# Kernel optimization log

Measured on AMD Instinct MI355X. Metric: run time of the kernel, lower is better.

Reference implementation:

```python
import jax, jax.numpy as jnp
import numpy as np

MS = [1, 2, 4, 8, 16]          # args.ms_token_size
RESI = 0.5                     # Phi resi_ratio
# PhiPartiallyShared: 4 phis, ticks = linspace(1/(2*4)... wait K==4 -> linspace(1/3/K, 1-1/3/K, K)
_TICKS = np.linspace(1.0 / 3.0 / 4.0, 1.0 - 1.0 / 3.0 / 4.0, 4)
PHI_IDX = [int(np.argmin(np.abs(_TICKS - (si / (len(MS) - 1))))) for si in range(len(MS))]


def _phi(h, w, b):
    # Phi.forward: h*(1-r) + conv3x3(h)*r
    c = jax.lax.conv_general_dilated(h, w, (1, 1), 'SAME',
                                     dimension_numbers=('NCHW', 'OIHW', 'NCHW'))
    c = c + b[None, :, None, None]
    return h * (1.0 - RESI) + c * RESI


def _area_down(z, ph, pw):
    # F.interpolate mode='area' with integer ratio == block mean
    B, C, H, W = z.shape
    return z.reshape(B, C, ph, H // ph, pw, W // pw).mean(axis=(3, 5))


def setup_inputs() -> dict:
    key = jax.random.key(0)
    k1, k2, k3 = jax.random.split(key, 3)
    B, C, H, W = 32, 64, 16, 16
    K = 8192
    f = jax.random.normal(k1, (B, C, H, W), dtype=jnp.float32)
    # nn.Embedding init: uniform(-1/K, 1/K)
    emb_w = jax.random.uniform(k2, (K, C), dtype=jnp.float32,
                               minval=-1.0 / K, maxval=1.0 / K)
    phi_w = jax.random.normal(k3, (4, C, C, 3, 3), dtype=jnp.float32) * 0.02
    phi_b = jnp.zeros((4, C), dtype=jnp.float32)
    return {'f': f, 'emb_w': emb_w, 'phi_w': phi_w, 'phi_b': phi_b}


def reference(f, emb_w, phi_w, phi_b):
    B, C, H, W = f.shape
    f = jax.lax.stop_gradient(f)  # z_enc.detach()
    z_rest = f
    f_hat = jnp.zeros_like(f)
    w_sq = jnp.sum(emb_w * emb_w, axis=1)  # [K]
    for si, pn in enumerate(MS):
        last = (si == len(MS) - 1)
        z = z_rest if last else _area_down(z_rest, pn, pn)
        zf = z.transpose(0, 2, 3, 1).reshape(-1, C)  # [B*pn*pn, C]
        # ||z||^2 + ||w||^2 - 2 z.w  (matches square-sum + addmm)
        d = jnp.sum(zf * zf, axis=1, keepdims=True) + w_sq[None, :] \
            - 2.0 * (zf @ emb_w.T)
        tok = jnp.argmin(d, axis=1)                  # [B*pn*pn]
        h = emb_w[tok].reshape(B, pn, pn, C).transpose(0, 3, 1, 2)
        if not last:
            h = jax.image.resize(h, (B, C, H, W), method='cubic')
        h = _phi(h, phi_w[PHI_IDX[si]], phi_b[PHI_IDX[si]])
        f_hat = f_hat + h
        z_rest = z_rest - h
    return f_hat
```

## Files before the change

### kernel.cpp

```cpp
#include <hip/hip_runtime.h>
#include <math.h>
#include <float.h>

#define BB 32
#define CC 64
#define KK 8192
#define NPIX 256
#define NELEM (BB*CC*NPIX)

typedef unsigned short u16;
typedef __attribute__((ext_vector_type(8))) short bf16x8;
typedef __attribute__((ext_vector_type(4))) float f32x4;

__device__ __forceinline__ u16 f2bf(float v) {
  unsigned u = __float_as_uint(v);
  return (u16)((u + 0x7FFFu + ((u >> 16) & 1u)) >> 16);
}

__global__ void k_prep(const float* __restrict__ f, float* __restrict__ zr,
                       float* __restrict__ out, const float* __restrict__ emb,
                       float* __restrict__ wsq32, u16* __restrict__ ehi) {
  int i = blockIdx.x * 256 + threadIdx.x;
  if (i < NELEM) { zr[i] = f[i]; out[i] = 0.f; ehi[i] = f2bf(emb[i]); }
  if (i < KK) {
    const float* row = emb + i * 64;
    double s = 0.0;
    #pragma unroll
    for (int c = 0; c < 64; ++c) s += (double)row[c] * (double)row[c];
    wsq32[i] = (float)s;
  }
}

__global__ void k_down(const float* __restrict__ zr, float* __restrict__ zd, int pn) {
#pragma clang fp contract(off)
  int i = blockIdx.x * 256 + threadIdx.x;
  int pnpn = pn * pn;
  int n = BB * CC * pnpn;
  if (i >= n) return;
  int x = i % pn; int y = (i / pn) % pn; int bc = i / pnpn;
  int bs = 16 / pn;
  const float* src = zr + bc * NPIX + (y * bs) * 16 + x * bs;
  float acc = 0.f;
  for (int dy = 0; dy < bs; ++dy) {
    const float* a = src + dy * 16;
    float s;
    if (bs == 16) {
      float r[8];
      #pragma unroll
      for (int j = 0; j < 8; ++j) r[j] = a[j] + a[8 + j];
      s = ((r[0] + r[1]) + (r[2] + r[3])) + ((r[4] + r[5]) + (r[6] + r[7]));
    } else if (bs == 8) {
      s = ((a[0] + a[1]) + (a[2] + a[3])) + ((a[4] + a[5]) + (a[6] + a[7]));
    } else if (bs == 4) {
      s = ((a[0] + a[1]) + a[2]) + a[3];
    } else {
      s = a[0] + a[1];
    }
    acc = acc + s;
  }
  zd[i] = acc * (1.f / (bs * bs));
}

__global__ __launch_bounds__(256) void k_pack(
    const float* __restrict__ zr, int pn, int bs,
    u16* __restrict__ zhi, float* __restrict__ zt32, float* __restrict__ zsq32) {
#pragma clang fp contract(off)
  int tid = threadIdx.x;
  int lv = tid >> 6, c = tid & 63;
  int vec = blockIdx.x * 4 + lv;
  int pnpn = pn * pn;
  int b = vec / pnpn, p = vec % pnpn;
  int y = p / pn, x = p % pn;
  const float* src = zr + ((size_t)(b * 64 + c)) * 256 + (y * bs) * 16 + x * bs;
  float v;
  if (bs == 1) {
    v = src[0];
  } else {
    v = (src[0] + src[1]) + (src[16] + src[17]);
    v = v * 0.25f;
  }
  zhi[(size_t)vec * 64 + c] = f2bf(v);
  zt32[(size_t)vec * 64 + c] = v;
  double sq = (double)v * (double)v;
  #pragma unroll
  for (int m = 1; m < 64; m <<= 1)
    sq += __shfl_xor(sq, m, 64);
  if (c == 0) zsq32[vec] = (float)sq;
}

__global__ __launch_bounds__(256, 4) void k_argmin(
    const float* __restrict__ zd, const float* __restrict__ emb,
    const float* __restrict__ wsq32,
    float* __restrict__ pd, int* __restrict__ pi,
    int numVec, int pnpn, int kchunk) {
#pragma clang fp contract(off)
  __shared__ __align__(16) float zt[32][68];
  __shared__ __align__(16) float et[64 * 64];
  __shared__ float ws_s[64];
  __shared__ float red_d[256];
  __shared__ int   red_i[256];
  int tid = threadIdx.x;
  int v0 = blockIdx.x * 32;
  int kbase = blockIdx.y * kchunk;

  for (int idx = tid; idx < 32 * 64; idx += 256) {
    int v = idx >> 6, c = idx & 63;
    int vi = v0 + v;
    float val = 0.f;
    if (vi < numVec) {
      int b = vi / pnpn, p = vi % pnpn;
      val = zd[(b * 64 + c) * pnpn + p];
    }
    zt[v][c] = val;
  }
  __syncthreads();

  const int v = tid & 31, kg = tid >> 5;
  float4 z4[16];
  #pragma unroll
  for (int i = 0; i < 16; ++i) z4[i] = *reinterpret_cast<float4*>(&zt[v][i * 4]);
  float zsq = 0.f;
  #pragma unroll
  for (int i = 0; i < 16; ++i)
    zsq += z4[i].x * z4[i].x + z4[i].y * z4[i].y + z4[i].z * z4[i].z + z4[i].w * z4[i].w;

  float bd = FLT_MAX; int bi = 0x7fffffff;
  for (int k0 = 0; k0 < kchunk; k0 += 64) {
    __syncthreads();
    {
      const float4* gsrc = reinterpret_cast<const float4*>(emb + (size_t)(kbase + k0) * 64);
      float4* ldst = reinterpret_cast<float4*>(et);
      #pragma unroll
      for (int idx = 0; idx < 4; ++idx)
        ldst[tid + idx * 256] = gsrc[tid + idx * 256];
    }
    if (tid < 64) ws_s[tid] = wsq32[kbase + k0 + tid];
    __syncthreads();
    #pragma unroll
    for (int j = 0; j < 8; ++j) {
      int kl = kg * 8 + j;
      const float4* e4 = reinterpret_cast<const float4*>(&et[kl * 64]);
      float acc = 0.f;
      #pragma unroll
      for (int i = 0; i < 16; ++i) {
        float4 e = e4[i];
        acc = __builtin_fmaf(z4[i].x, e.x, acc);
        acc = __builtin_fmaf(z4[i].y, e.y, acc);
        acc = __builtin_fmaf(z4[i].z, e.z, acc);
        acc = __builtin_fmaf(z4[i].w, e.w, acc);
      }
      float t1 = zsq + ws_s[kl];
      float d  = t1 - 2.0f * acc;
      if (d < bd) { bd = d; bi = kbase + k0 + kl; }
    }
  }
  red_d[tid] = bd; red_i[tid] = bi;
  __syncthreads();
  if (tid < 32) {
    float fb = red_d[tid]; int fi = red_i[tid];
    #pragma unroll
    for (int g = 1; g < 8; ++g) {
      float cd = red_d[g * 32 + tid]; int ci = red_i[g * 32 + tid];
      if (cd < fb || (cd == fb && ci < fi)) { fb = cd; fi = ci; }
    }
    int vi = v0 + tid;
    if (vi < numVec) {
      pd[blockIdx.y * numVec + vi] = fb;
      pi[blockIdx.y * numVec + vi] = fi;
    }
  }
}

__global__ __launch_bounds__(256, 8) void k_argmin_mfma(
    const u16* __restrict__ zhi, const u16* __restrict__ ehi,
    const float* __restrict__ wsq32, float* __restrict__ cdp,
    int numVec, int part) {
  __shared__ u16  es[2][64 * 72];
  __shared__ float wss[2][64];
  const int tid = threadIdx.x;
  const int wid = tid >> 6, lane = tid & 63;
  const int l15 = lane & 15, l4 = lane >> 4;
  const int vw = blockIdx.x * 128 + wid * 32;
  const int kbase = blockIdx.y * part;
  const int KSx = gridDim.y;

  bf16x8 za[2][2];
  #pragma unroll
  for (int s = 0; s < 2; ++s) {
    const u16* zp = zhi + (size_t)(vw + s * 16 + l15) * 64 + l4 * 8;
    za[s][0] = *reinterpret_cast<const bf16x8*>(zp);
    za[s][1] = *reinterpret_cast<const bf16x8*>(zp + 32);
  }

  float d1[2][4], d2[2][4];
  #pragma unroll
  for (int s = 0; s < 2; ++s)
    #pragma unroll
    for (int r = 0; r < 4; ++r) { d1[s][r] = -FLT_MAX; d2[s][r] = -FLT_MAX; }

  const int NT = part >> 6;
  #define STAGE(buf, t)                                                      \
    { const u16* src = ehi + (size_t)(kbase + (t) * 64) * 64;                \
      int code = tid >> 2, seg = tid & 3;                                    \
      const bf16x8* s8 = reinterpret_cast<const bf16x8*>(src + code * 64 + seg * 16); \
      bf16x8 v0 = s8[0], v1 = s8[1];                                         \
      bf16x8* d8 = reinterpret_cast<bf16x8*>(&es[buf][code * 72 + seg * 16]);\
      d8[0] = v0; d8[1] = v1;                                                \
      if (tid < 64) wss[buf][tid] = wsq32[kbase + (t) * 64 + tid]; }

  STAGE(0, 0);
  __syncthreads();
  for (int t = 0; t < NT; ++t) {
    int cur = t & 1;
    if (t + 1 < NT) { STAGE(cur ^ 1, t + 1); }
    #pragma unroll
    for (int ct = 0; ct < 4; ++ct) {
      const u16* eb = &es[cur][(ct * 16 + l15) * 72 + l4 * 8];
      bf16x8 b0 = *reinterpret_cast<const bf16x8*>(eb);
      bf16x8 b1 = *reinterpret_cast<const bf16x8*>(eb + 32);
      float hwl = -0.5f * wss[cur][ct * 16 + l15];
      unsigned idu = (unsigned)(t * 64 + ct * 16 + l15);
      #pragma unroll
      for (int s = 0; s < 2; ++s) {
        f32x4 acc = {hwl, hwl, hwl, hwl};
        acc = __builtin_amdgcn_mfma_f32_16x16x32_bf16(za[s][0], b0, acc, 0, 0, 0);
        acc = __builtin_amdgcn_mfma_f32_16x16x32_bf16(za[s][1], b1, acc, 0, 0, 0);
        #pragma unroll
        for (int r = 0; r < 4; ++r) {
          float key = __uint_as_float((__float_as_uint(acc[r]) & 0xFFFFFF00u) | idu);
          float o1 = d1[s][r];
          d1[s][r] = fmaxf(o1, key);
          d2[s][r] = __builtin_amdgcn_fmed3f(o1, key, d2[s][r]);
        }
      }
    }
    __syncthreads();
  }

  #pragma unroll
  for (int s = 0; s < 2; ++s)
    #pragma unroll
    for (int r = 0; r < 4; ++r) {
      float q0 = d1[s][r], q1 = d2[s][r];
      #pragma unroll
      for (int m = 1; m < 8; m <<= 1) {
        float p0 = __shfl_xor(q0, m), p1 = __shfl_xor(q1, m);
        { bool c0 = p0 > q0, c1 = p0 > q1;
          q1 = c0 ? q0 : (c1 ? p0 : q1);
          q0 = c0 ? p0 : q0; }
        { bool c0 = p1 > q0, c1 = p1 > q1;
          q1 = c0 ? q0 : (c1 ? p1 : q1);
          q0 = c0 ? p1 : q0; }
      }
      if ((l15 & 7) == 0) {
        int vec = vw + s * 16 + l4 * 4 + r;
        int half = l15 >> 3;
        size_t base = ((size_t)vec * KSx + blockIdx.y) * 4 + half * 2;
        cdp[base + 0] = q0; cdp[base + 1] = q1;
      }
    }
}

__global__ __launch_bounds__(256) void k_rescore(
    const float* __restrict__ cdp, const float* __restrict__ zt32,
    const float* __restrict__ emb, const float* __restrict__ wsq32,
    const float* __restrict__ zsq32,
    float* __restrict__ pd, int* __restrict__ pi,
    int numVec, int ncand) {
#pragma clang fp contract(off)
  __shared__ float zsh[4][64];
  int tid = threadIdx.x;
  int wid = tid >> 6, lane = tid & 63;
  int v0 = blockIdx.x * 4;
  zsh[wid][lane] = zt32[(size_t)v0 * 64 + tid];
  __syncthreads();

  int vec = v0 + wid;
  float zsq = zsq32[vec];
  const float* cdb = cdp + (size_t)vec * ncand;
  float dv0 = cdb[lane];
  float dv1 = (ncand > 64) ? cdb[lane + 64] : -FLT_MAX;
  int j0 = lane, j1 = lane + 64;
  int ki0 = ((j0 >> 2) << 8) | (int)(__float_as_uint(dv0) & 0xFFu);
  int ki1 = ((j1 >> 2) << 8) | (int)(__float_as_uint(dv1) & 0xFFu);

  float amax = fmaxf(dv0, dv1);
  #pragma unroll
  for (int m = 1; m < 64; m <<= 1) amax = fmaxf(amax, __shfl_xor(amax, m, 64));
  float thr = amax - 0.5f * fmaf(sqrtf(zsq), 1.25e-5f, 1e-4f);

  const float* zw = zsh[wid];
  float d = FLT_MAX; int bi = 0x7fffffff;
  #pragma unroll
  for (int slot = 0; slot < 2; ++slot) {
    float dv = slot ? dv1 : dv0;
    int   kk = slot ? ki1 : ki0;
    if (dv >= thr) {
      const float4* er = reinterpret_cast<const float4*>(emb + (size_t)kk * 64);
      float4 e4[16];
      #pragma unroll
      for (int i = 0; i < 16; ++i) e4[i] = er[i];
      float acc = 0.f;
      #pragma unroll
      for (int i = 0; i < 16; ++i) {
        acc = __builtin_fmaf(zw[4 * i + 0], e4[i].x, acc);
        acc = __builtin_fmaf(zw[4 * i + 1], e4[i].y, acc);
        acc = __builtin_fmaf(zw[4 * i + 2], e4[i].z, acc);
        acc = __builtin_fmaf(zw[4 * i + 3], e4[i].w, acc);
      }
      float t1 = zsq + wsq32[kk];
      float dd = t1 - 2.0f * acc;
      if (dd < d || (dd == d && kk < bi)) { d = dd; bi = kk; }
    }
  }
  #pragma unroll
  for (int m = 1; m < 64; m <<= 1) {
    float od = __shfl_xor(d, m, 64);
    int   oi = __shfl_xor(bi, m, 64);
    if (od < d || (od == d && oi < bi)) { d = od; bi = oi; }
  }
  if (lane == 0) { pd[vec] = 0.f; pi[vec] = bi; }
}

__global__ __launch_bounds__(256) void k_up(
    const float* __restrict__ pd, const int* __restrict__ pi,
    const float* __restrict__ emb, float* __restrict__ hup,
    int pn, int ksplit) {
  __shared__ float td[256];
  __shared__ int   ti[256];
  __shared__ int   tok_s[256];
  __shared__ float wsh[16][4];
  __shared__ int   i0sh[16];

  int t = threadIdx.x;
  int i = blockIdx.x * 256 + t;
  int p = i & 255; int c = (i >> 8) & 63; int b = i >> 14;
  int P = pn * pn;
  int numVec = BB * P;
  int R = 256 / P;
  int v = t % P, sg = t / P;

  float bd = FLT_MAX; int bi = 0x7fffffff;
  for (int s = sg; s < ksplit; s += R) {
    float cd = pd[s * numVec + b * P + v]; int ci = pi[s * numVec + b * P + v];
    if (cd < bd || (cd == bd && ci < bi)) { bd = cd; bi = ci; }
  }
  td[t] = bd; ti[t] = bi;
  __syncthreads();
  for (int r = R >> 1; r >= 1; r >>= 1) {
    if (sg < r) {
      float cd = td[t + r * P]; int ci = ti[t + r * P];
      if (cd < td[t] || (cd == td[t] && ci < ti[t])) { td[t] = cd; ti[t] = ci; }
    }
    __syncthreads();
  }
  if (t < P) tok_s[t] = ti[t];
  if (pn < 16 && t < 16) {
    double s = (t + 0.5) * ((double)pn / 16.0) - 0.5;
    int i0 = (int)floor(s) - 1;
    int hi = pn - 4; if (hi < 0) hi = 0;
    if (i0 < 0) i0 = 0; if (i0 > hi) i0 = hi;
    double wv[4]; double sum = 0.0;
    #pragma unroll
    for (int qq = 0; qq < 4; ++qq) {
      int ii = i0 + qq;
      double w = 0.0;
      if (ii < pn) {
        double xx = fabs(s - (double)ii);
        if (xx < 1.0)       w = ((1.5 * xx - 2.5) * xx) * xx + 1.0;
        else if (xx < 2.0)  w = ((-0.5 * xx + 2.5) * xx - 4.0) * xx + 2.0;
      }
      wv[qq] = w; sum += w;
    }
    i0sh[t] = i0;
    #pragma unroll
    for (int qq = 0; qq < 4; ++qq) wsh[t][qq] = (float)(wv[qq] / sum);
  }
  __syncthreads();

  if (pn == 16) { hup[i] = emb[(size_t)tok_s[p] * 64 + c]; return; }

  int y = p >> 4, x = p & 15;
  int iy0 = i0sh[y], ix0 = i0sh[x];
  float acc = 0.f;
  #pragma unroll
  for (int ty = 0; ty < 4; ++ty) {
    float wy = wsh[y][ty];
    int iy = iy0 + ty; if (iy > pn - 1) iy = pn - 1;
    float tmp = 0.f;
    #pragma unroll
    for (int tx = 0; tx < 4; ++tx) {
      float wx = wsh[x][tx];
      int ix = ix0 + tx; if (ix > pn - 1) ix = pn - 1;
      tmp += wx * emb[(size_t)tok_s[iy * pn + ix] * 64 + c];
    }
    acc += wy * tmp;
  }
  hup[i] = acc;
}

__global__ __launch_bounds__(256) void k_conv(
    const float* __restrict__ hup, const float* __restrict__ w,
    const float* __restrict__ bias, float* __restrict__ out, float* __restrict__ zr) {
  __shared__ __align__(16) float ins[16][18 * 18];
  __shared__ __align__(16) float wsh[8 * 64 * 12];
  int tid = threadIdx.x;
  int b = blockIdx.x;
  int ocb = blockIdx.y;

  for (int idx = tid; idx < 16 * 324; idx += 256)
    (&ins[0][0])[idx] = 0.f;
  for (int idx = tid; idx < 8 * 64 * 9; idx += 256) {
    int ocic = idx / 9, t = idx - ocic * 9;
    wsh[ocic * 12 + t] = w[(size_t)ocb * 8 * 64 * 9 + idx];
  }

  const int wid = tid >> 6, lane = tid & 63;
  const int ocg = wid >> 1;
  const int ph = (wid & 1) * 64 + lane;
  const int x = ph & 15, y2 = ph >> 4;

  float acc[4][2];
  #pragma unroll
  for (int j = 0; j < 4; ++j) {
    float bv = bias[ocb * 8 + ocg * 4 + j];
    acc[j][0] = bv; acc[j][1] = bv;
  }

  const float* hb = hup + (size_t)b * 64 * NPIX;
  float sreg[16];
  #pragma unroll
  for (int r = 0; r < 16; ++r) sreg[r] = hb[r * 256 + tid];

  for (int cc = 0; cc < 4; ++cc) {
    __syncthreads();
    #pragma unroll
    for (int r = 0; r < 16; ++r) {
      int idx = r * 256 + tid;
      int icl = idx >> 8, p = idx & 255;
      ins[icl][((p >> 4) + 1) * 18 + (p & 15) + 1] = sreg[r];
    }
    __syncthreads();
    if (cc < 3) {
      #pragma unroll
      for (int r = 0; r < 16; ++r) sreg[r] = hb[(cc + 1) * 4096 + r * 256 + tid];
    }

    #pragma unroll 2
    for (int icl = 0; icl < 16; ++icl) {
      float vt[4][3];
      const float* ip = &ins[icl][y2 * 2 * 18 + x];
      #pragma unroll
      for (int r = 0; r < 4; ++r)
        #pragma unroll
        for (int cxx = 0; cxx < 3; ++cxx)
          vt[r][cxx] = ip[r * 18 + cxx];

      int ic = cc * 16 + icl;
      #pragma unroll
      for (int j = 0; j < 4; ++j) {
        const float* wp = &wsh[((ocg * 4 + j) * 64 + ic) * 12];
        float4 wa = *reinterpret_cast<const float4*>(wp);
        float4 wb = *reinterpret_cast<const float4*>(wp + 4);
        float w8 = wp[8];
        float wv[9] = {wa.x, wa.y, wa.z, wa.w, wb.x, wb.y, wb.z, wb.w, w8};
        float a0 = acc[j][0], a1 = acc[j][1];
        #pragma unroll
        for (int dy = 0; dy < 3; ++dy)
          #pragma unroll
          for (int dx = 0; dx < 3; ++dx) {
            float wt = wv[dy * 3 + dx];
            a0 = __builtin_fmaf(vt[dy][dx], wt, a0);
            a1 = __builtin_fmaf(vt[dy + 1][dx], wt, a1);
          }
        acc[j][0] = a0; acc[j][1] = a1;
      }
    }
  }

  #pragma unroll
  for (int j = 0; j < 4; ++j) {
    int oc = ocb * 8 + ocg * 4 + j;
    #pragma unroll
    for (int r = 0; r < 2; ++r) {
      size_t gi = ((size_t)b * 64 + oc) * NPIX + (y2 * 2 + r) * 16 + x;
      float h = hup[gi];
      float ho = 0.5f * h + 0.5f * acc[j][r];
      out[gi] += ho;
      zr[gi]  -= ho;
    }
  }
}

extern "C" void kernel_launch(void* const* d_in, const int* in_sizes, int n_in,
                              void* d_out, int out_size, void* d_ws, size_t ws_size,
                              hipStream_t stream) {
  const float* f    = (const float*)d_in[0];
  const float* emb  = (const float*)d_in[1];
  const float* phiw = (const float*)d_in[2];
  const float* phib = (const float*)d_in[3];
  float* out = (float*)d_out;

  float* ws  = (float*)d_ws;
  float* zr     = ws;
  float* zd     = ws + 524288;
  float* hup    = ws + 557056;
  float* wsq32  = ws + 1081344;
  float* pd     = ws + 1089536;
  int*   pi     = (int*)(ws + 1097728);
  u16*   zhi    = (u16*)(ws + 1105920);
  u16*   ehi    = (u16*)(ws + 1368064);
  float* cand_d = ws + 1630208;
  float* zsq32  = ws + 2678784;
  float* zt32   = ws + 2686976;

  double start = 1.0 / 3.0 / 4.0;
  double stop  = 1.0 - 1.0 / 3.0 / 4.0;
  double step  = (stop - start) / 3.0;
  double ticks[4] = { start, 1.0 * step + start, 2.0 * step + start, stop };
  int phi_idx[5];
  for (int si = 0; si < 5; ++si) {
    double xx = si / 4.0;
    int bj = 0; double bdd = fabs(ticks[0] - xx);
    for (int j = 1; j < 4; ++j) { double dd = fabs(ticks[j] - xx); if (dd < bdd) { bdd = dd; bj = j; } }
    phi_idx[si] = bj;
  }

  static const int MSarr[5] = {1, 2, 4, 8, 16};

  k_prep<<<NELEM / 256, 256, 0, stream>>>(f, zr, out, emb, wsq32, ehi);

  const int KS[5] = {128, 32, 16, 32, 32};
  for (int si = 0; si < 5; ++si) {
    int pn = MSarr[si], pnpn = pn * pn, numVec = BB * pnpn;
    int ksplit = KS[si];
    if (si >= 3) {
      int bs = 16 / pn;
      int part = KK / ksplit;
      k_pack<<<numVec / 4, 256, 0, stream>>>(zr, pn, bs, zhi, zt32, zsq32);
      dim3 g(numVec / 128, ksplit);
      k_argmin_mfma<<<g, 256, 0, stream>>>(zhi, ehi, wsq32, cand_d, numVec, part);
      k_rescore<<<numVec / 4, 256, 0, stream>>>(cand_d, zt32, emb,
                                                wsq32, zsq32, pd, pi,
                                                numVec, ksplit * 4);
      k_up<<<NELEM / 256, 256, 0, stream>>>(pd, pi, emb, hup, pn, 1);
    } else {
      int n = BB * CC * pnpn;
      k_down<<<(n + 255) / 256, 256, 0, stream>>>(zr, zd, pn);
      int kchunk = KK / ksplit;
      dim3 g((numVec + 31) / 32, ksplit);
      k_argmin<<<g, 256, 0, stream>>>(zd, emb, wsq32, pd, pi, numVec, pnpn, kchunk);
      k_up<<<NELEM / 256, 256, 0, stream>>>(pd, pi, emb, hup, pn, ksplit);
    }
    int pidx = phi_idx[si];
    k_conv<<<dim3(BB, 8), 256, 0, stream>>>(hup, phiw + pidx * 64 * 64 * 9,
                                            phib + pidx * 64, out, zr);
  }
}
```

Before: 312.0 us.

## Route scale 4 through MFMA argmin path and overlap codebook tile loads with compute

Extends k_pack to handle 4x4 block averaging so scale index 2 (pn=4) can use the bf16 MFMA argmin plus fp32 rescore path instead of the scalar fp32 argmin kernel, with a larger k-split for that scale. The MFMA argmin staging is split into a global load into registers issued before the compute loop and an LDS write after it. This hides global-memory latency behind the MFMA work. It costs extra registers, and routing pn=4 through the bf16 candidate path depends on the top-2 rescore preserving exact argmin results.

```diff
diff --git a/kernel.cpp b/kernel.cpp
--- a/kernel.cpp
+++ b/kernel.cpp
@@ -75,9 +75,18 @@
   float v;
   if (bs == 1) {
     v = src[0];
-  } else {
+  } else if (bs == 2) {
     v = (src[0] + src[1]) + (src[16] + src[17]);
     v = v * 0.25f;
+  } else {
+    float acc = 0.f;
+    #pragma unroll
+    for (int dy = 0; dy < 4; ++dy) {
+      const float* a = src + dy * 16;
+      float s = ((a[0] + a[1]) + a[2]) + a[3];
+      acc = acc + s;
+    }
+    v = acc * 0.0625f;
   }
   zhi[(size_t)vec * 64 + c] = f2bf(v);
   zt32[(size_t)vec * 64 + c] = v;
@@ -199,20 +208,24 @@
     for (int r = 0; r < 4; ++r) { d1[s][r] = -FLT_MAX; d2[s][r] = -FLT_MAX; }
 
   const int NT = part >> 6;
-  #define STAGE(buf, t)                                                      \
-    { const u16* src = ehi + (size_t)(kbase + (t) * 64) * 64;                \
-      int code = tid >> 2, seg = tid & 3;                                    \
-      const bf16x8* s8 = reinterpret_cast<const bf16x8*>(src + code * 64 + seg * 16); \
-      bf16x8 v0 = s8[0], v1 = s8[1];                                         \
-      bf16x8* d8 = reinterpret_cast<bf16x8*>(&es[buf][code * 72 + seg * 16]);\
-      d8[0] = v0; d8[1] = v1;                                                \
-      if (tid < 64) wss[buf][tid] = wsq32[kbase + (t) * 64 + tid]; }
-
-  STAGE(0, 0);
+  bf16x8 r0, r1; float wreg = 0.f;
+  const int scode = tid >> 2, sseg = tid & 3;
+
+  #define LOADT(t)                                                           \
+    { const bf16x8* s8 = reinterpret_cast<const bf16x8*>(                    \
+          ehi + (size_t)(kbase + (t) * 64) * 64 + scode * 64 + sseg * 16);   \
+      r0 = s8[0]; r1 = s8[1];                                                \
+      if (tid < 64) wreg = wsq32[kbase + (t) * 64 + tid]; }
+  #define WRITET(buf)                                                        \
+    { bf16x8* d8 = reinterpret_cast<bf16x8*>(&es[buf][scode * 72 + sseg * 16]); \
+      d8[0] = r0; d8[1] = r1;                                                \
+      if (tid < 64) wss[buf][tid] = wreg; }
+
+  LOADT(0); WRITET(0);
   __syncthreads();
   for (int t = 0; t < NT; ++t) {
     int cur = t & 1;
-    if (t + 1 < NT) { STAGE(cur ^ 1, t + 1); }
+    if (t + 1 < NT) LOADT(t + 1);
     #pragma unroll
     for (int ct = 0; ct < 4; ++ct) {
       const u16* eb = &es[cur][(ct * 16 + l15) * 72 + l4 * 8];
@@ -234,6 +247,7 @@
         }
       }
     }
+    if (t + 1 < NT) WRITET(cur ^ 1);
     __syncthreads();
   }
 
@@ -530,11 +544,11 @@
 
   k_prep<<<NELEM / 256, 256, 0, stream>>>(f, zr, out, emb, wsq32, ehi);
 
-  const int KS[5] = {128, 32, 16, 32, 32};
+  const int KS[5] = {128, 32, 32, 32, 32};
   for (int si = 0; si < 5; ++si) {
     int pn = MSarr[si], pnpn = pn * pn, numVec = BB * pnpn;
     int ksplit = KS[si];
-    if (si >= 3) {
+    if (si >= 2) {
       int bs = 16 / pn;
       int part = KK / ksplit;
       k_pack<<<numVec / 4, 256, 0, stream>>>(zr, pn, bs, zhi, zt32, zsq32);
```

New measurement: 368.1 us. 18.0% more time.
